# Kernel optimization log

Hardware: AMD Instinct MI355X
Metric: run time of the kernel (lower is better)

The kernel has to match this reference:

```python
import math
import jax, jax.numpy as jnp
import numpy as np

H = 16          # n_heads
WIN = 512       # window_size (causal, one-sided)
BS = 64         # block_size


def setup_inputs() -> dict:
    key = jax.random.key(0)
    ks = jax.random.split(key, 5)
    B, T, D = 2, 4096, 1024
    x = jax.random.normal(ks[0], (B, T, D), dtype=jnp.float32)
    init = 0.02
    Wq = jax.random.normal(ks[1], (D, D), dtype=jnp.float32) * init
    Wk = jax.random.normal(ks[2], (D, D), dtype=jnp.float32) * init
    Wv = jax.random.normal(ks[3], (D, D), dtype=jnp.float32) * init
    Wo = jax.random.normal(ks[4], (D, D), dtype=jnp.float32) * init
    return {"x": x, "Wq": Wq, "Wk": Wk, "Wv": Wv, "Wo": Wo}


def _sliding_window_attn(q, k, v):
    """Causal sliding-window attention, banded/block-sparse form.

    q,k,v: (B, H, T, hd). Only key blocks within the window of each query
    block are gathered, honoring the sparsity the torch mask encodes.
    """
    B, Hn, T, hd = q.shape
    nb = T // BS                   # number of blocks
    nw1 = WIN // BS + 1            # key blocks touching a query block
    scale = 1.0 / math.sqrt(hd)

    qb = q.reshape(B, Hn, nb, BS, hd)
    kb = k.reshape(B, Hn, nb, BS, hd)
    vb = v.reshape(B, Hn, nb, BS, hd)

    offs = jnp.arange(-(WIN // BS), 1)                 # (nw1,)
    idx_raw = jnp.arange(nb)[:, None] + offs[None, :]  # (nb, nw1)
    idx = jnp.clip(idx_raw, 0, nb - 1)

    kg = jnp.take(kb, idx, axis=2)   # (B,H,nb,nw1,BS,hd)
    vg = jnp.take(vb, idx, axis=2)

    scores = jnp.einsum('bhnqd,bhnwkd->bhnqwk', qb, kg) * scale

    qpos = (jnp.arange(nb) * BS)[:, None, None, None] + jnp.arange(BS)[None, :, None, None]  # (nb,BS,1,1)
    kpos = (idx_raw * BS)[:, None, :, None] + jnp.arange(BS)[None, None, None, :]            # (nb,1,nw1,BS)
    valid = (idx_raw[:, None, :, None] >= 0) & (kpos <= qpos) & (qpos - kpos < WIN)
    scores = jnp.where(valid[None, None], scores, -1e9)

    p = jax.nn.softmax(scores.reshape(B, Hn, nb, BS, nw1 * BS), axis=-1)
    p = p.reshape(B, Hn, nb, BS, nw1, BS)
    out = jnp.einsum('bhnqwk,bhnwkd->bhnqd', p, vg)
    return out.reshape(B, Hn, T, hd)


def reference(x, Wq, Wk, Wv, Wo):
    B, T, D = x.shape
    hd = D // H

    def proj(W):  # torch Linear: x @ W.T
        return (x @ W.T).reshape(B, T, H, hd).transpose(0, 2, 1, 3)

    q, k, v = proj(Wq), proj(Wk), proj(Wv)
    out = _sliding_window_attn(q, k, v)            # (B,H,T,hd)
    out = out.transpose(0, 2, 1, 3).reshape(B, T, D)
    return out @ Wo.T
```

## Files before the change

### kernel.cpp

```cpp
#include <hip/hip_runtime.h>

#define DI static __device__ __forceinline__

typedef __attribute__((ext_vector_type(8))) short short8;
typedef __attribute__((ext_vector_type(4))) float f32x4;

DI unsigned short f2bf(float f) {
    union { float f; unsigned int u; } v; v.f = f;
    unsigned int r = v.u + 0x7FFFu + ((v.u >> 16) & 1u);
    return (unsigned short)(r >> 16);
}

DI void gload_lds16(const void* g, void* l) {
    __builtin_amdgcn_global_load_lds(
        (const __attribute__((address_space(1))) void*)g,
        (__attribute__((address_space(3))) void*)l, 16, 0, 0);
}

DI short8 ldsfrag(const void* base, int row, int bytecol) {
    return *(const short8*)((const char*)base + row * 128 + (bytecol ^ ((row & 7) << 4)));
}

__global__ __launch_bounds__(256) void k_cvt(
    const float* __restrict__ x, const float* __restrict__ wq,
    const float* __restrict__ wk, const float* __restrict__ wv,
    const float* __restrict__ wo,
    unsigned short* __restrict__ xb, unsigned short* __restrict__ wqb,
    unsigned short* __restrict__ wkb, unsigned short* __restrict__ wvb,
    unsigned short* __restrict__ wob)
{
    const float* src; unsigned short* dst; int n;
    switch (blockIdx.y) {
        case 0:  src = x;  dst = xb;  n = 8388608; break;
        case 1:  src = wq; dst = wqb; n = 1048576; break;
        case 2:  src = wk; dst = wkb; n = 1048576; break;
        case 3:  src = wv; dst = wvb; n = 1048576; break;
        default: src = wo; dst = wob; n = 1048576; break;
    }
    int idx = (blockIdx.x * 256 + threadIdx.x) * 4;
    if (idx >= n) return;
    float4 v = *(const float4*)(src + idx);
    unsigned long long o = (unsigned long long)f2bf(v.x)
        | ((unsigned long long)f2bf(v.y) << 16)
        | ((unsigned long long)f2bf(v.z) << 32)
        | ((unsigned long long)f2bf(v.w) << 48);
    *(unsigned long long*)(dst + idx) = o;
}

DI void gemm_core(const unsigned short* __restrict__ Ag,
                  const unsigned short* __restrict__ Bg,
                  int m0, int n0, char* smem, f32x4 acc[4][4])
{
    const int t = threadIdx.x, lane = t & 63;
    const int wid = t >> 6, wr = wid >> 2, wc = wid & 3;
    const int kl = lane & 15, hi = lane >> 4;

#pragma unroll
    for (int m = 0; m < 4; ++m)
#pragma unroll
        for (int n = 0; n < 4; ++n)
            acc[m][n] = f32x4{0.f, 0.f, 0.f, 0.f};

    const int ca  = t,       ra  = ca  >> 2, sa  = ((ca  & 3) ^ ((ra  >> 1) & 3)) * 8;
    const int cb0 = t,       rb0 = cb0 >> 2, sb0 = ((cb0 & 3) ^ ((rb0 >> 1) & 3)) * 8;
    const int cb1 = t + 512, rb1 = cb1 >> 2, sb1 = ((cb1 & 3) ^ ((rb1 >> 1) & 3)) * 8;
    const unsigned short* pa  = Ag + (long)(m0 + ra)  * 1024 + sa;
    const unsigned short* pb0 = Bg + (long)(n0 + rb0) * 1024 + sb0;
    const unsigned short* pb1 = Bg + (long)(n0 + rb1) * 1024 + sb1;

#define STAGE(TILE, BUF) do {                                          \
        char* _sb = smem + (BUF) * 24576;                              \
        gload_lds16(pa  + (TILE) * 32, _sb + ca * 16);                 \
        gload_lds16(pb0 + (TILE) * 32, _sb + 8192 + cb0 * 16);         \
        gload_lds16(pb1 + (TILE) * 32, _sb + 8192 + cb1 * 16);         \
    } while (0)

    STAGE(0, 0);
    STAGE(1, 1);

    const int swz = ((hi ^ ((kl >> 1) & 3)) << 4);
    const int aoff = (wr * 64 + kl) * 64 + swz;
    const int boff = 8192 + (wc * 64 + kl) * 64 + swz;

#define KSTEP(KS, CUR, PRE, ISSUE, VM) do {                                   \
        asm volatile("s_waitcnt vmcnt(" VM ")" ::: "memory");                 \
        __builtin_amdgcn_s_barrier();                                         \
        __builtin_amdgcn_sched_barrier(0);                                    \
        if (ISSUE) STAGE((KS) + 2, PRE);                                      \
        const char* _ab = smem + (CUR) * 24576 + aoff;                        \
        const char* _bb = smem + (CUR) * 24576 + boff;                        \
        short8 _fa[4], _fb[4];                                                \
        _Pragma("unroll")                                                     \
        for (int m = 0; m < 4; ++m) _fa[m] = *(const short8*)(_ab + m * 1024);\
        _Pragma("unroll")                                                     \
        for (int n = 0; n < 4; ++n) _fb[n] = *(const short8*)(_bb + n * 1024);\
        __builtin_amdgcn_s_setprio(1);                                        \
        _Pragma("unroll")                                                     \
        for (int m = 0; m < 4; ++m)                                           \
        _Pragma("unroll")                                                     \
            for (int n = 0; n < 4; ++n)                                       \
                acc[m][n] = __builtin_amdgcn_mfma_f32_16x16x32_bf16(          \
                    _fa[m], _fb[n], acc[m][n], 0, 0, 0);                      \
        __builtin_amdgcn_s_setprio(0);                                        \
    } while (0)

    for (int u = 0; u < 10; ++u) {
        const int ks = u * 3;
        KSTEP(ks + 0, 0, 2, 1, "3");
        KSTEP(ks + 1, 1, 0, 1, "3");
        KSTEP(ks + 2, 2, 1, 1, "3");
    }
    KSTEP(30, 0, 2, 0, "3");
    KSTEP(31, 1, 0, 0, "0");
#undef KSTEP
#undef STAGE
}

__global__ __launch_bounds__(512, 4) void k_gemm_qkv(
    const unsigned short* __restrict__ xb,
    const unsigned short* __restrict__ wqb, const unsigned short* __restrict__ wkb,
    const unsigned short* __restrict__ wvb,
    unsigned short* __restrict__ Qo, unsigned short* __restrict__ Ko,
    unsigned short* __restrict__ Vo)
{
    extern __shared__ char smem[];
    const int bx = blockIdx.x, by = blockIdx.y;
    const int w = by >> 2, nb = by & 3;
    const unsigned short* Bw = (w == 0) ? wqb : ((w == 1) ? wkb : wvb);
    unsigned short* Ow = (w == 0) ? Qo : ((w == 1) ? Ko : Vo);
    const float sc = (w == 0) ? 0.125f : 1.0f;

    f32x4 acc[4][4];
    gemm_core(xb, Bw, bx * 128, nb * 256, smem, acc);

    const int t = threadIdx.x, lane = t & 63, wid = t >> 6;
    const int wr = wid >> 2, wc = wid & 3, kl = lane & 15, hi = lane >> 4;
    const int h = nb * 4 + wc;
#pragma unroll
    for (int m = 0; m < 4; ++m)
#pragma unroll
        for (int r = 0; r < 4; ++r) {
            int grow = bx * 128 + wr * 64 + m * 16 + hi * 4 + r;
            int bi = grow >> 12, tt = grow & 4095;
            unsigned short* rowp = Ow + ((long)(bi * 16 + h) * 4096 + tt) * 64;
#pragma unroll
            for (int n = 0; n < 4; ++n)
                rowp[n * 16 + kl] = f2bf(acc[m][n][r] * sc);
        }
}

__global__ __launch_bounds__(256) void k_vtrans(const unsigned short* __restrict__ V,
                                                unsigned short* __restrict__ VT)
{
    __shared__ unsigned short S[64 * 64];
    const int t = threadIdx.x;
    const int bh = blockIdx.y, tb = blockIdx.x;
    const unsigned short* src = V + ((long)bh * 4096 + tb * 64) * 64;
    unsigned short* dst = VT + (long)bh * 4096 * 64 + tb * 64;
    char* sb = (char*)S;
#pragma unroll
    for (int c = t; c < 512; c += 256) {
        int r = c >> 3, o8 = (c & 7) * 8;
        *(uint4*)(sb + r * 128 + ((o8 * 2) ^ (((r >> 3) & 7) << 4))) =
            *(const uint4*)(src + r * 64 + o8);
    }
    __syncthreads();
#pragma unroll
    for (int c = t; c < 512; c += 256) {
        int d = c >> 3, t0 = (c & 7) * 8;
        uint4 val;
        unsigned short* pv = (unsigned short*)&val;
#pragma unroll
        for (int jj = 0; jj < 8; ++jj) {
            int row = t0 + jj;
            pv[jj] = *(const unsigned short*)(sb + row * 128 +
                        ((d * 2) ^ (((row >> 3) & 7) << 4)));
        }
        *(uint4*)(dst + (long)d * 4096 + t0) = val;
    }
}

__global__ __launch_bounds__(256) void k_attn(
    const unsigned short* __restrict__ Q, const unsigned short* __restrict__ K,
    const unsigned short* __restrict__ VT, unsigned short* __restrict__ AO)
{
    __shared__ unsigned short Qs[4096];
    __shared__ unsigned short Ks[2][4096], Vs[2][4096];
    const int t = threadIdx.x, lane = t & 63, wid = t >> 6;
    const int kl = lane & 15, hi = lane >> 4;
    const int bid = blockIdx.x;
    const int sid = (bid & 7) * 256 + (bid >> 3);
    const int i = sid & 63, bh = sid >> 6;
    const int b = bh >> 4, h = bh & 15;
    const char* qg = (const char*)(Q + ((long)bh * 4096 + i * 64) * 64);
    const char* kg = (const char*)(K + (long)bh * 4096 * 64);
    const char* vg = (const char*)(VT + (long)bh * 64 * 4096);

    const int c0 = t, c1 = t + 256;
    const int r0 = c0 >> 3, sw0 = ((c0 & 7) * 16) ^ ((r0 & 7) << 4);
    const int r1 = c1 >> 3, sw1 = ((c1 & 7) * 16) ^ ((r1 & 7) << 4);
    const char* kg0 = kg + r0 * 128 + sw0;
    const char* kg1 = kg + r1 * 128 + sw1;
    const char* vg0 = vg + r0 * 8192 + sw0;
    const char* vg1 = vg + r1 * 8192 + sw1;

    const int j0 = (i >= 8) ? i - 8 : 0;

    gload_lds16(qg + r0 * 128 + sw0, (char*)Qs + c0 * 16);
    gload_lds16(qg + r1 * 128 + sw1, (char*)Qs + c1 * 16);
    gload_lds16(kg0 + j0 * 8192, (char*)Ks[0] + c0 * 16);
    gload_lds16(kg1 + j0 * 8192, (char*)Ks[0] + c1 * 16);
    gload_lds16(vg0 + j0 * 128,  (char*)Vs[0] + c0 * 16);
    gload_lds16(vg1 + j0 * 128,  (char*)Vs[0] + c1 * 16);
    __syncthreads();

    short8 aq[2];
    aq[0] = ldsfrag(Qs, wid * 16 + kl, hi * 16);
    aq[1] = ldsfrag(Qs, wid * 16 + kl, 64 + hi * 16);

    float lsum[4] = {0.f, 0.f, 0.f, 0.f};
    f32x4 o[4];
#pragma unroll
    for (int nt = 0; nt < 4; ++nt) o[nt] = f32x4{0.f, 0.f, 0.f, 0.f};

    const int qrow = wid * 16 + hi * 4;
    char* pw = (char*)Qs + wid * 2048;

    for (int j = j0; j <= i; ++j) {
        const int buf = (j - j0) & 1;
        if (j < i) {
            const int nb = buf ^ 1;
            gload_lds16(kg0 + (j + 1) * 8192, (char*)Ks[nb] + c0 * 16);
            gload_lds16(kg1 + (j + 1) * 8192, (char*)Ks[nb] + c1 * 16);
            gload_lds16(vg0 + (j + 1) * 128,  (char*)Vs[nb] + c0 * 16);
            gload_lds16(vg1 + (j + 1) * 128,  (char*)Vs[nb] + c1 * 16);
        }

        f32x4 s[4];
#pragma unroll
        for (int nt = 0; nt < 4; ++nt) {
            s[nt] = f32x4{0.f, 0.f, 0.f, 0.f};
#pragma unroll
            for (int kk = 0; kk < 2; ++kk)
                s[nt] = __builtin_amdgcn_mfma_f32_16x16x32_bf16(
                    aq[kk], ldsfrag(Ks[buf], nt * 16 + kl, kk * 64 + hi * 16),
                    s[nt], 0, 0, 0);
        }

        if (j == i) {
#pragma unroll
            for (int nt = 0; nt < 4; ++nt) {
                int key = nt * 16 + kl;
#pragma unroll
                for (int r = 0; r < 4; ++r)
                    if (key > qrow + r) s[nt][r] = -1e9f;
            }
        } else if (i - j == 8) {
#pragma unroll
            for (int nt = 0; nt < 4; ++nt) {
                int key = nt * 16 + kl;
#pragma unroll
                for (int r = 0; r < 4; ++r)
                    if (key <= qrow + r) s[nt][r] = -1e9f;
            }
        }

#pragma unroll
        for (int nt = 0; nt < 4; ++nt)
#pragma unroll
            for (int r = 0; r < 4; ++r) {
                float p = __expf(s[nt][r]);
                s[nt][r] = p;
                lsum[r] += p;
            }

#pragma unroll
        for (int nt = 0; nt < 4; ++nt)
#pragma unroll
            for (int r = 0; r < 4; ++r) {
                int q = hi * 4 + r;
                int colb = (nt * 16 + kl) * 2;
                *(unsigned short*)(pw + q * 128 + (colb ^ ((q & 7) << 4))) =
                    f2bf(s[nt][r]);
            }

        short8 pa0 = ldsfrag(pw, kl, hi * 16);
        short8 pa1 = ldsfrag(pw, kl, 64 + hi * 16);
#pragma unroll
        for (int nt = 0; nt < 4; ++nt) {
            o[nt] = __builtin_amdgcn_mfma_f32_16x16x32_bf16(
                pa0, ldsfrag(Vs[buf], nt * 16 + kl, hi * 16), o[nt], 0, 0, 0);
            o[nt] = __builtin_amdgcn_mfma_f32_16x16x32_bf16(
                pa1, ldsfrag(Vs[buf], nt * 16 + kl, 64 + hi * 16), o[nt], 0, 0, 0);
        }

        __syncthreads();
    }

#pragma unroll
    for (int d = 1; d < 16; d <<= 1)
#pragma unroll
        for (int r = 0; r < 4; ++r) lsum[r] += __shfl_xor(lsum[r], d);

    float inv[4];
#pragma unroll
    for (int r = 0; r < 4; ++r) inv[r] = 1.0f / lsum[r];
#pragma unroll
    for (int r = 0; r < 4; ++r) {
        int tt = i * 64 + wid * 16 + hi * 4 + r;
        unsigned short* rowp = AO + ((long)(b * 4096 + tt)) * 1024 + h * 64;
#pragma unroll
        for (int nt = 0; nt < 4; ++nt)
            rowp[nt * 16 + kl] = f2bf(o[nt][r] * inv[r]);
    }
}

__global__ __launch_bounds__(512, 4) void k_gemm_out(
    const unsigned short* __restrict__ AO, const unsigned short* __restrict__ wob,
    float* __restrict__ out)
{
    extern __shared__ char smem[];
    const int bx = blockIdx.x, nb = blockIdx.y;
    f32x4 acc[4][4];
    gemm_core(AO, wob, bx * 128, nb * 256, smem, acc);

    const int t = threadIdx.x, lane = t & 63, wid = t >> 6;
    const int wr = wid >> 2, wc = wid & 3, kl = lane & 15, hi = lane >> 4;
#pragma unroll
    for (int m = 0; m < 4; ++m)
#pragma unroll
        for (int r = 0; r < 4; ++r) {
            int grow = bx * 128 + wr * 64 + m * 16 + hi * 4 + r;
            float* rowp = out + (long)grow * 1024 + nb * 256 + wc * 64;
#pragma unroll
            for (int n = 0; n < 4; ++n)
                rowp[n * 16 + kl] = acc[m][n][r];
        }
}

extern "C" void kernel_launch(void* const* d_in, const int* in_sizes, int n_in,
                              void* d_out, int out_size, void* d_ws, size_t ws_size,
                              hipStream_t stream) {
    const float* x  = (const float*)d_in[0];
    const float* wq = (const float*)d_in[1];
    const float* wk = (const float*)d_in[2];
    const float* wv = (const float*)d_in[3];
    const float* wo = (const float*)d_in[4];

    char* ws = (char*)d_ws;
    const size_t MB = 1024 * 1024;
    unsigned short* xb  = (unsigned short*)(ws);
    unsigned short* wqb = (unsigned short*)(ws + 16 * MB);
    unsigned short* wkb = (unsigned short*)(ws + 18 * MB);
    unsigned short* wvb = (unsigned short*)(ws + 20 * MB);
    unsigned short* wob = (unsigned short*)(ws + 22 * MB);
    unsigned short* Qp  = (unsigned short*)(ws + 24 * MB);
    unsigned short* Kp  = (unsigned short*)(ws + 40 * MB);
    unsigned short* Vp  = (unsigned short*)(ws + 56 * MB);
    unsigned short* VTp = (unsigned short*)(ws + 72 * MB);
    unsigned short* AOp = xb;

    hipFuncSetAttribute((const void*)k_gemm_qkv,
                        hipFuncAttributeMaxDynamicSharedMemorySize, 73728);
    hipFuncSetAttribute((const void*)k_gemm_out,
                        hipFuncAttributeMaxDynamicSharedMemorySize, 73728);

    dim3 blk(256);
    k_cvt<<<dim3(8192, 5), blk, 0, stream>>>(x, wq, wk, wv, wo,
                                             xb, wqb, wkb, wvb, wob);
    k_gemm_qkv<<<dim3(64, 12), 512, 73728, stream>>>(xb, wqb, wkb, wvb,
                                                     Qp, Kp, Vp);
    k_vtrans<<<dim3(64, 32), blk, 0, stream>>>(Vp, VTp);
    k_attn<<<2048, blk, 0, stream>>>(Qp, Kp, VTp, AOp);
    k_gemm_out<<<dim3(64, 4), 512, 73728, stream>>>(AOp, wob, (float*)d_out);
}
```

Measured before the change: 148.4 us.

## Use 4 waves with 128x64 warp tiles in GEMM core instead of 8 waves

The GEMM block drops from 512 to 256 threads, and each wave now computes a 128x64 output tile (8x4 MFMA fragments) instead of 64x64. Each thread issues twice as many global-to-LDS loads per stage, and the vmcnt waits are adjusted to match. The aim is more MFMA work per LDS fragment load, since the B fragments are reused across 8 rows, and fewer waves contending at barriers. The cost is doubled accumulator registers, which caps occupancy at 2 blocks per CU, and less latency hiding from fewer waves.

```diff
diff --git a/kernel.cpp b/kernel.cpp
--- a/kernel.cpp
+++ b/kernel.cpp
@@ -49,37 +49,46 @@
 
 DI void gemm_core(const unsigned short* __restrict__ Ag,
                   const unsigned short* __restrict__ Bg,
-                  int m0, int n0, char* smem, f32x4 acc[4][4])
+                  int m0, int n0, char* smem, f32x4 acc[8][4])
 {
     const int t = threadIdx.x, lane = t & 63;
-    const int wid = t >> 6, wr = wid >> 2, wc = wid & 3;
+    const int wc = t >> 6;
     const int kl = lane & 15, hi = lane >> 4;
 
 #pragma unroll
-    for (int m = 0; m < 4; ++m)
+    for (int m = 0; m < 8; ++m)
 #pragma unroll
         for (int n = 0; n < 4; ++n)
             acc[m][n] = f32x4{0.f, 0.f, 0.f, 0.f};
 
-    const int ca  = t,       ra  = ca  >> 2, sa  = ((ca  & 3) ^ ((ra  >> 1) & 3)) * 8;
+    const int ca0 = t,       ra0 = ca0 >> 2, sa0 = ((ca0 & 3) ^ ((ra0 >> 1) & 3)) * 8;
+    const int ca1 = t + 256, ra1 = ca1 >> 2, sa1 = ((ca1 & 3) ^ ((ra1 >> 1) & 3)) * 8;
     const int cb0 = t,       rb0 = cb0 >> 2, sb0 = ((cb0 & 3) ^ ((rb0 >> 1) & 3)) * 8;
-    const int cb1 = t + 512, rb1 = cb1 >> 2, sb1 = ((cb1 & 3) ^ ((rb1 >> 1) & 3)) * 8;
-    const unsigned short* pa  = Ag + (long)(m0 + ra)  * 1024 + sa;
+    const int cb1 = t + 256, rb1 = cb1 >> 2, sb1 = ((cb1 & 3) ^ ((rb1 >> 1) & 3)) * 8;
+    const int cb2 = t + 512, rb2 = cb2 >> 2, sb2 = ((cb2 & 3) ^ ((rb2 >> 1) & 3)) * 8;
+    const int cb3 = t + 768, rb3 = cb3 >> 2, sb3 = ((cb3 & 3) ^ ((rb3 >> 1) & 3)) * 8;
+    const unsigned short* pa0 = Ag + (long)(m0 + ra0) * 1024 + sa0;
+    const unsigned short* pa1 = Ag + (long)(m0 + ra1) * 1024 + sa1;
     const unsigned short* pb0 = Bg + (long)(n0 + rb0) * 1024 + sb0;
     const unsigned short* pb1 = Bg + (long)(n0 + rb1) * 1024 + sb1;
+    const unsigned short* pb2 = Bg + (long)(n0 + rb2) * 1024 + sb2;
+    const unsigned short* pb3 = Bg + (long)(n0 + rb3) * 1024 + sb3;
 
 #define STAGE(TILE, BUF) do {                                          \
         char* _sb = smem + (BUF) * 24576;                              \
-        gload_lds16(pa  + (TILE) * 32, _sb + ca * 16);                 \
+        gload_lds16(pa0 + (TILE) * 32, _sb + ca0 * 16);                \
+        gload_lds16(pa1 + (TILE) * 32, _sb + ca1 * 16);                \
         gload_lds16(pb0 + (TILE) * 32, _sb + 8192 + cb0 * 16);         \
-        gload_lds16(pb1 + (TILE) * 32, _sb + 8192 + cb1 * 16);         \
+        gload_lds16(pb1 + (TILE) * 32, _sb + 8192 + cb1 * 16);        \
+        gload_lds16(pb2 + (TILE) * 32, _sb + 8192 + cb2 * 16);        \
+        gload_lds16(pb3 + (TILE) * 32, _sb + 8192 + cb3 * 16);        \
     } while (0)
 
     STAGE(0, 0);
     STAGE(1, 1);
 
     const int swz = ((hi ^ ((kl >> 1) & 3)) << 4);
-    const int aoff = (wr * 64 + kl) * 64 + swz;
+    const int aoff = kl * 64 + swz;
     const int boff = 8192 + (wc * 64 + kl) * 64 + swz;
 
 #define KSTEP(KS, CUR, PRE, ISSUE, VM) do {                                   \
@@ -89,14 +98,14 @@
         if (ISSUE) STAGE((KS) + 2, PRE);                                      \
         const char* _ab = smem + (CUR) * 24576 + aoff;                        \
         const char* _bb = smem + (CUR) * 24576 + boff;                        \
-        short8 _fa[4], _fb[4];                                                \
+        short8 _fa[8], _fb[4];                                                \
         _Pragma("unroll")                                                     \
-        for (int m = 0; m < 4; ++m) _fa[m] = *(const short8*)(_ab + m * 1024);\
+        for (int m = 0; m < 8; ++m) _fa[m] = *(const short8*)(_ab + m * 1024);\
         _Pragma("unroll")                                                     \
         for (int n = 0; n < 4; ++n) _fb[n] = *(const short8*)(_bb + n * 1024);\
         __builtin_amdgcn_s_setprio(1);                                        \
         _Pragma("unroll")                                                     \
-        for (int m = 0; m < 4; ++m)                                           \
+        for (int m = 0; m < 8; ++m)                                           \
         _Pragma("unroll")                                                     \
             for (int n = 0; n < 4; ++n)                                       \
                 acc[m][n] = __builtin_amdgcn_mfma_f32_16x16x32_bf16(          \
@@ -106,17 +115,17 @@
 
     for (int u = 0; u < 10; ++u) {
         const int ks = u * 3;
-        KSTEP(ks + 0, 0, 2, 1, "3");
-        KSTEP(ks + 1, 1, 0, 1, "3");
-        KSTEP(ks + 2, 2, 1, 1, "3");
-    }
-    KSTEP(30, 0, 2, 0, "3");
+        KSTEP(ks + 0, 0, 2, 1, "6");
+        KSTEP(ks + 1, 1, 0, 1, "6");
+        KSTEP(ks + 2, 2, 1, 1, "6");
+    }
+    KSTEP(30, 0, 2, 0, "6");
     KSTEP(31, 1, 0, 0, "0");
 #undef KSTEP
 #undef STAGE
 }
 
-__global__ __launch_bounds__(512, 4) void k_gemm_qkv(
+__global__ __launch_bounds__(256, 2) void k_gemm_qkv(
     const unsigned short* __restrict__ xb,
     const unsigned short* __restrict__ wqb, const unsigned short* __restrict__ wkb,
     const unsigned short* __restrict__ wvb,
@@ -130,17 +139,17 @@
     unsigned short* Ow = (w == 0) ? Qo : ((w == 1) ? Ko : Vo);
     const float sc = (w == 0) ? 0.125f : 1.0f;
 
-    f32x4 acc[4][4];
+    f32x4 acc[8][4];
     gemm_core(xb, Bw, bx * 128, nb * 256, smem, acc);
 
-    const int t = threadIdx.x, lane = t & 63, wid = t >> 6;
-    const int wr = wid >> 2, wc = wid & 3, kl = lane & 15, hi = lane >> 4;
+    const int t = threadIdx.x, lane = t & 63;
+    const int wc = t >> 6, kl = lane & 15, hi = lane >> 4;
     const int h = nb * 4 + wc;
 #pragma unroll
-    for (int m = 0; m < 4; ++m)
+    for (int m = 0; m < 8; ++m)
 #pragma unroll
         for (int r = 0; r < 4; ++r) {
-            int grow = bx * 128 + wr * 64 + m * 16 + hi * 4 + r;
+            int grow = bx * 128 + m * 16 + hi * 4 + r;
             int bi = grow >> 12, tt = grow & 4095;
             unsigned short* rowp = Ow + ((long)(bi * 16 + h) * 4096 + tt) * 64;
 #pragma unroll
@@ -315,22 +324,22 @@
     }
 }
 
-__global__ __launch_bounds__(512, 4) void k_gemm_out(
+__global__ __launch_bounds__(256, 2) void k_gemm_out(
     const unsigned short* __restrict__ AO, const unsigned short* __restrict__ wob,
     float* __restrict__ out)
 {
     extern __shared__ char smem[];
     const int bx = blockIdx.x, nb = blockIdx.y;
-    f32x4 acc[4][4];
+    f32x4 acc[8][4];
     gemm_core(AO, wob, bx * 128, nb * 256, smem, acc);
 
-    const int t = threadIdx.x, lane = t & 63, wid = t >> 6;
-    const int wr = wid >> 2, wc = wid & 3, kl = lane & 15, hi = lane >> 4;
-#pragma unroll
-    for (int m = 0; m < 4; ++m)
+    const int t = threadIdx.x, lane = t & 63;
+    const int wc = t >> 6, kl = lane & 15, hi = lane >> 4;
+#pragma unroll
+    for (int m = 0; m < 8; ++m)
 #pragma unroll
         for (int r = 0; r < 4; ++r) {
-            int grow = bx * 128 + wr * 64 + m * 16 + hi * 4 + r;
+            int grow = bx * 128 + m * 16 + hi * 4 + r;
             float* rowp = out + (long)grow * 1024 + nb * 256 + wc * 64;
 #pragma unroll
             for (int n = 0; n < 4; ++n)
@@ -368,9 +377,9 @@
     dim3 blk(256);
     k_cvt<<<dim3(8192, 5), blk, 0, stream>>>(x, wq, wk, wv, wo,
                                              xb, wqb, wkb, wvb, wob);
-    k_gemm_qkv<<<dim3(64, 12), 512, 73728, stream>>>(xb, wqb, wkb, wvb,
+    k_gemm_qkv<<<dim3(64, 12), 256, 73728, stream>>>(xb, wqb, wkb, wvb,
                                                      Qp, Kp, Vp);
     k_vtrans<<<dim3(64, 32), blk, 0, stream>>>(Vp, VTp);
     k_attn<<<2048, blk, 0, stream>>>(Qp, Kp, VTp, AOp);
-    k_gemm_out<<<dim3(64, 4), 512, 73728, stream>>>(AOp, wob, (float*)d_out);
-}
+    k_gemm_out<<<dim3(64, 4), 256, 73728, stream>>>(AOp, wob, (float*)d_out);
+}
```

New measurement: 148.3 us. No clear change (-0.1%).

## Fuse V transpose into QKV GEMM epilogue and flatten conversion grid

Applied to the files above, without the earlier changes.

The QKV projection GEMM now writes V directly in transposed (head, d, t) layout, which removes the separate k_vtrans kernel and its extra global read/write pass over V. The conversion kernel's grid also moves from a 2D launch with many idle blocks for the small weight tensors to an exact 1D launch. The transposed store scatters 2-byte writes with a 4096-element stride per lane, so those stores coalesce poorly and may cost more inside the GEMM epilogue.

```diff
diff --git a/kernel.cpp b/kernel.cpp
--- a/kernel.cpp
+++ b/kernel.cpp
@@ -29,22 +29,27 @@
     unsigned short* __restrict__ wkb, unsigned short* __restrict__ wvb,
     unsigned short* __restrict__ wob)
 {
-    const float* src; unsigned short* dst; int n;
-    switch (blockIdx.y) {
-        case 0:  src = x;  dst = xb;  n = 8388608; break;
-        case 1:  src = wq; dst = wqb; n = 1048576; break;
-        case 2:  src = wk; dst = wkb; n = 1048576; break;
-        case 3:  src = wv; dst = wvb; n = 1048576; break;
-        default: src = wo; dst = wob; n = 1048576; break;
-    }
     int idx = (blockIdx.x * 256 + threadIdx.x) * 4;
-    if (idx >= n) return;
-    float4 v = *(const float4*)(src + idx);
+    const float* src; unsigned short* dst; int off;
+    if (idx < 8388608) {
+        src = x; dst = xb; off = idx;
+    } else {
+        int rel = idx - 8388608;
+        int sel = rel >> 20;
+        off = rel & 1048575;
+        switch (sel) {
+            case 0:  src = wq; dst = wqb; break;
+            case 1:  src = wk; dst = wkb; break;
+            case 2:  src = wv; dst = wvb; break;
+            default: src = wo; dst = wob; break;
+        }
+    }
+    float4 v = *(const float4*)(src + off);
     unsigned long long o = (unsigned long long)f2bf(v.x)
         | ((unsigned long long)f2bf(v.y) << 16)
         | ((unsigned long long)f2bf(v.z) << 32)
         | ((unsigned long long)f2bf(v.w) << 48);
-    *(unsigned long long*)(dst + idx) = o;
+    *(unsigned long long*)(dst + off) = o;
 }
 
 DI void gemm_core(const unsigned short* __restrict__ Ag,
@@ -121,13 +126,12 @@
     const unsigned short* __restrict__ wqb, const unsigned short* __restrict__ wkb,
     const unsigned short* __restrict__ wvb,
     unsigned short* __restrict__ Qo, unsigned short* __restrict__ Ko,
-    unsigned short* __restrict__ Vo)
+    unsigned short* __restrict__ VTo)
 {
     extern __shared__ char smem[];
     const int bx = blockIdx.x, by = blockIdx.y;
     const int w = by >> 2, nb = by & 3;
     const unsigned short* Bw = (w == 0) ? wqb : ((w == 1) ? wkb : wvb);
-    unsigned short* Ow = (w == 0) ? Qo : ((w == 1) ? Ko : Vo);
     const float sc = (w == 0) ? 0.125f : 1.0f;
 
     f32x4 acc[4][4];
@@ -136,47 +140,34 @@
     const int t = threadIdx.x, lane = t & 63, wid = t >> 6;
     const int wr = wid >> 2, wc = wid & 3, kl = lane & 15, hi = lane >> 4;
     const int h = nb * 4 + wc;
-#pragma unroll
-    for (int m = 0; m < 4; ++m)
-#pragma unroll
-        for (int r = 0; r < 4; ++r) {
-            int grow = bx * 128 + wr * 64 + m * 16 + hi * 4 + r;
-            int bi = grow >> 12, tt = grow & 4095;
-            unsigned short* rowp = Ow + ((long)(bi * 16 + h) * 4096 + tt) * 64;
-#pragma unroll
-            for (int n = 0; n < 4; ++n)
-                rowp[n * 16 + kl] = f2bf(acc[m][n][r] * sc);
-        }
-}
-
-__global__ __launch_bounds__(256) void k_vtrans(const unsigned short* __restrict__ V,
-                                                unsigned short* __restrict__ VT)
-{
-    __shared__ unsigned short S[64 * 64];
-    const int t = threadIdx.x;
-    const int bh = blockIdx.y, tb = blockIdx.x;
-    const unsigned short* src = V + ((long)bh * 4096 + tb * 64) * 64;
-    unsigned short* dst = VT + (long)bh * 4096 * 64 + tb * 64;
-    char* sb = (char*)S;
-#pragma unroll
-    for (int c = t; c < 512; c += 256) {
-        int r = c >> 3, o8 = (c & 7) * 8;
-        *(uint4*)(sb + r * 128 + ((o8 * 2) ^ (((r >> 3) & 7) << 4))) =
-            *(const uint4*)(src + r * 64 + o8);
-    }
-    __syncthreads();
-#pragma unroll
-    for (int c = t; c < 512; c += 256) {
-        int d = c >> 3, t0 = (c & 7) * 8;
-        uint4 val;
-        unsigned short* pv = (unsigned short*)&val;
-#pragma unroll
-        for (int jj = 0; jj < 8; ++jj) {
-            int row = t0 + jj;
-            pv[jj] = *(const unsigned short*)(sb + row * 128 +
-                        ((d * 2) ^ (((row >> 3) & 7) << 4)));
-        }
-        *(uint4*)(dst + (long)d * 4096 + t0) = val;
+
+    if (w < 2) {
+        unsigned short* Ow = (w == 0) ? Qo : Ko;
+#pragma unroll
+        for (int m = 0; m < 4; ++m)
+#pragma unroll
+            for (int r = 0; r < 4; ++r) {
+                int grow = bx * 128 + wr * 64 + m * 16 + hi * 4 + r;
+                int bi = grow >> 12, tt = grow & 4095;
+                unsigned short* rowp = Ow + ((long)(bi * 16 + h) * 4096 + tt) * 64;
+#pragma unroll
+                for (int n = 0; n < 4; ++n)
+                    rowp[n * 16 + kl] = f2bf(acc[m][n][r] * sc);
+            }
+    } else {
+#pragma unroll
+        for (int m = 0; m < 4; ++m)
+#pragma unroll
+            for (int r = 0; r < 4; ++r) {
+                int grow = bx * 128 + wr * 64 + m * 16 + hi * 4 + r;
+                int bi = grow >> 12, tt = grow & 4095;
+                unsigned short* hb = VTo + (long)(bi * 16 + h) * 262144;
+#pragma unroll
+                for (int n = 0; n < 4; ++n) {
+                    int d = n * 16 + kl;
+                    hb[(long)d * 4096 + tt] = f2bf(acc[m][n][r]);
+                }
+            }
     }
 }
 
@@ -356,8 +347,7 @@
     unsigned short* wob = (unsigned short*)(ws + 22 * MB);
     unsigned short* Qp  = (unsigned short*)(ws + 24 * MB);
     unsigned short* Kp  = (unsigned short*)(ws + 40 * MB);
-    unsigned short* Vp  = (unsigned short*)(ws + 56 * MB);
-    unsigned short* VTp = (unsigned short*)(ws + 72 * MB);
+    unsigned short* VTp = (unsigned short*)(ws + 56 * MB);
     unsigned short* AOp = xb;
 
     hipFuncSetAttribute((const void*)k_gemm_qkv,
@@ -366,11 +356,10 @@
                         hipFuncAttributeMaxDynamicSharedMemorySize, 73728);
 
     dim3 blk(256);
-    k_cvt<<<dim3(8192, 5), blk, 0, stream>>>(x, wq, wk, wv, wo,
-                                             xb, wqb, wkb, wvb, wob);
+    k_cvt<<<12288, blk, 0, stream>>>(x, wq, wk, wv, wo,
+                                     xb, wqb, wkb, wvb, wob);
     k_gemm_qkv<<<dim3(64, 12), 512, 73728, stream>>>(xb, wqb, wkb, wvb,
-                                                     Qp, Kp, Vp);
-    k_vtrans<<<dim3(64, 32), blk, 0, stream>>>(Vp, VTp);
+                                                     Qp, Kp, VTp);
     k_attn<<<2048, blk, 0, stream>>>(Qp, Kp, VTp, AOp);
     k_gemm_out<<<dim3(64, 4), 512, 73728, stream>>>(AOp, wob, (float*)d_out);
 }
```

After: 138.4 us. 1.07x faster.
